# Performance work log

Measured on AMD Instinct MI355X. Metric: run time of the kernel, lower is better.

Reference implementation:

```python
import jax, jax.numpy as jnp
import numpy as np
import math

PERIODS = [4, 2, 1]          # period_num[-3:] sorted desc
SEQ, PRED, CH = 192, 96, 8
TOPM, DM = 20, 512
N_TRAIN, BSZ = 10000, 32


def decompose_mg(data):
    # data: [N, L, C] -> mg: [P, N, L, C], offset-removed (last step per period)
    N, L, C = data.shape
    mgs = []
    for g in PERIODS:
        cur = data.reshape(N, L // g, g, C).mean(axis=2)   # pooled
        cur = jnp.repeat(cur, g, axis=1)                   # repeat_interleave
        mgs.append(cur)
    mg = jnp.stack(mgs, axis=0)                            # [P, N, L, C]
    offset = mg[:, :, -1:, :]
    return mg - offset


def l2norm(x, eps=1e-12):
    n = jnp.sqrt(jnp.sum(x * x, axis=-1, keepdims=True))
    return x / jnp.maximum(n, eps)


def setup_inputs() -> dict:
    key = jax.random.key(0)
    ks = jax.random.split(key, 10)
    F = SEQ * CH
    return {
        "x": jax.random.normal(ks[0], (BSZ, SEQ, CH), dtype=jnp.float32),
        "index": jax.random.randint(ks[1], (BSZ,), 0, N_TRAIN),
        "train_data_all": jax.random.normal(ks[2], (N_TRAIN, SEQ, CH), dtype=jnp.float32),
        "y_data_all": jax.random.normal(ks[3], (N_TRAIN, PRED, CH), dtype=jnp.float32),
        "W_sim": jax.random.normal(ks[4], (F, F), dtype=jnp.float32) / math.sqrt(F),
        "b_sim": jax.random.normal(ks[5], (F,), dtype=jnp.float32) * 0.01,
        "Wq": jax.random.normal(ks[6], (CH, DM), dtype=jnp.float32) / math.sqrt(CH),
        "bq": jax.random.normal(ks[7], (DM,), dtype=jnp.float32) * 0.01,
        "Wk": jax.random.normal(ks[8], (CH, DM), dtype=jnp.float32) / math.sqrt(CH),
        "bk": jax.random.normal(ks[9], (DM,), dtype=jnp.float32) * 0.01,
    }


def reference(x, index, train_data_all, y_data_all, W_sim, b_sim, Wq, bq, Wk, bk):
    P = len(PERIODS)
    bsz = x.shape[0]
    n_train = train_data_all.shape[0]

    # multi-period decomposition (prepare_dataset + retrieve)
    train_mg = decompose_mg(train_data_all)   # [P, N, SEQ, CH]
    y_mg = decompose_mg(y_data_all)           # [P, N, PRED, CH]
    x_mg = decompose_mg(x)                    # [P, B, SEQ, CH]

    # periodic_batch_corr: shared linear then cosine similarity
    bx = x_mg.reshape(P, bsz, -1) @ W_sim + b_sim           # [P, B, F]
    ax = train_mg.reshape(P, n_train, -1) @ W_sim + b_sim   # [P, N, F]
    sim = jnp.einsum('pbf,pnf->pbn', l2norm(bx), l2norm(ax))

    # self-exclusion sliding mask (train=True)
    win = 2 * (SEQ + PRED) - 1
    slid = jnp.arange(win)[None, :] + (index - SEQ - PRED + 1)[:, None]
    slid = jnp.clip(slid, 0, n_train - 1)
    mask = jnp.zeros((bsz, n_train), dtype=bool).at[
        jnp.arange(bsz)[:, None], slid].set(True)
    sim = jnp.where(mask[None], -jnp.inf, sim)

    # top-m retrieval
    _, topm_idx = jax.lax.top_k(sim, TOPM)                  # [P, B, TOPM]

    # gather neighbors per period
    gather = jax.vmap(lambda src, i: src[i])                # over period axis
    k = gather(train_mg, topm_idx)                          # [P, B, M, SEQ, CH]
    v = gather(y_mg, topm_idx)                              # [P, B, M, PRED, CH]

    # cross attention (shared projections across periods)
    q_emb = x_mg @ Wq + bq                                  # [P, B, S, D]
    k_emb = k @ Wk + bk                                     # [P, B, M, T, D]
    scores = jnp.einsum('pbsd,pbmtd->pbsmt', q_emb, k_emb) / math.sqrt(DM)
    S = scores.shape[2]
    w = jax.nn.softmax(scores.reshape(P, bsz, S, TOPM * S), axis=-1)
    w = w.reshape(P, bsz, S, TOPM, S)
    nw = w.sum(axis=-1).sum(axis=2)                         # [P, B, M]
    nw = jax.nn.softmax(nw, axis=-1)
    out = jnp.einsum('pbm,pbmlc->pblc', nw, v)              # [P, B, PRED, CH]
    return out
```

## Files before the change

kernel.cpp:

```cpp
#include <hip/hip_runtime.h>
#include <hip/hip_bf16.h>
#include <math.h>

#define NPER 3
#define SEQL 192
#define PREDL 96
#define CH 8
#define FD 1536
#define NT 10000
#define BS 32
#define PB 96
#define TOPM 20
#define DM 512
#define HALFW 287
#define NROWS 30000
#define NRP2 10112
#define NRB2 79
#define NCB 12
#define PCOLS 24
#define NWG2 (NRB2*NCB)
#define NJ 3840
#define K0R 384
#define K1R 768
#define K2R 1536
#define KS 16
#define KSD 8
#define RSQRT_DM 0.04419417382415922f

typedef __attribute__((ext_vector_type(8))) short bf16x8;
typedef __attribute__((ext_vector_type(4))) float f32x4;
typedef __attribute__((address_space(3))) short lds_short_t;
typedef __attribute__((address_space(1))) const short glb_short_t;

__device__ inline float bflo(unsigned u){ return __uint_as_float(u << 16); }
__device__ inline float bfhi(unsigned u){ return __uint_as_float(u & 0xFFFF0000u); }
__device__ inline float bf2f(unsigned short u){ return __uint_as_float((unsigned)u << 16); }
__device__ inline unsigned short f2bf(float v){
  __hip_bfloat16 h = __float2bfloat16(v);
  return *reinterpret_cast<unsigned short*>(&h);
}

template<int L>
__global__ __launch_bounds__(256) void k_decompose(const float* __restrict__ data,
                                                   float* __restrict__ mg,
                                                   __hip_bfloat16* __restrict__ m0,
                                                   __hip_bfloat16* __restrict__ m1,
                                                   __hip_bfloat16* __restrict__ m2,
                                                   int N) {
  __shared__ float row[L*CH];
  __shared__ float m4[(L/4)*CH];
  __shared__ float m2s[(L/2)*CH];
  int n = blockIdx.x;
  const float* src = data + (size_t)n*L*CH;
  for (int e = threadIdx.x; e < L*CH/4; e += 256)
    *reinterpret_cast<float4*>(&row[e*4]) = *reinterpret_cast<const float4*>(&src[e*4]);
  __syncthreads();
  for (int i = threadIdx.x; i < (L/4)*CH; i += 256) {
    int j = i >> 3, c = i & 7;
    m4[i] = (row[(4*j)*CH+c] + row[(4*j+1)*CH+c] + row[(4*j+2)*CH+c] + row[(4*j+3)*CH+c]) * 0.25f;
  }
  for (int i = threadIdx.x; i < (L/2)*CH; i += 256) {
    int j = i >> 3, c = i & 7;
    m2s[i] = (row[(2*j)*CH+c] + row[(2*j+1)*CH+c]) * 0.5f;
  }
  __syncthreads();
  if (mg) {
    size_t plane = (size_t)N*L*CH;
    size_t base  = (size_t)n*L*CH;
    for (int e = threadIdx.x; e < L*CH/4; e += 256) {
      int i = e*4;
      int l = i >> 3, c0 = i & 7;
      float v0[4], v1[4], v2[4];
      #pragma unroll
      for (int j=0;j<4;j++) {
        int c = c0 + j;
        v0[j] = m4[(l>>2)*CH+c] - m4[(L/4-1)*CH+c];
        v1[j] = m2s[(l>>1)*CH+c] - m2s[(L/2-1)*CH+c];
        v2[j] = row[i+j] - row[(L-1)*CH+c];
      }
      *reinterpret_cast<float4*>(&mg[base+i])           = make_float4(v0[0],v0[1],v0[2],v0[3]);
      *reinterpret_cast<float4*>(&mg[plane+base+i])     = make_float4(v1[0],v1[1],v1[2],v1[3]);
      *reinterpret_cast<float4*>(&mg[2*plane+base+i])   = make_float4(v2[0],v2[1],v2[2],v2[3]);
    }
  }
  if (m0) {
    unsigned short* p0 = (unsigned short*)m0 + (size_t)n*K0R;
    unsigned short* p1 = (unsigned short*)m1 + (size_t)n*K1R;
    unsigned short* p2 = (unsigned short*)m2 + (size_t)n*K2R;
    for (int e = threadIdx.x; e < K0R/4; e += 256) {
      int i = e*4, c0 = i & 7;
      ushort4 u;
      u.x = f2bf(m4[i]   - m4[(L/4-1)*CH + c0]);
      u.y = f2bf(m4[i+1] - m4[(L/4-1)*CH + c0+1]);
      u.z = f2bf(m4[i+2] - m4[(L/4-1)*CH + c0+2]);
      u.w = f2bf(m4[i+3] - m4[(L/4-1)*CH + c0+3]);
      *reinterpret_cast<ushort4*>(&p0[i]) = u;
    }
    for (int e = threadIdx.x; e < K1R/4; e += 256) {
      int i = e*4, c0 = i & 7;
      ushort4 u;
      u.x = f2bf(m2s[i]   - m2s[(L/2-1)*CH + c0]);
      u.y = f2bf(m2s[i+1] - m2s[(L/2-1)*CH + c0+1]);
      u.z = f2bf(m2s[i+2] - m2s[(L/2-1)*CH + c0+2]);
      u.w = f2bf(m2s[i+3] - m2s[(L/2-1)*CH + c0+3]);
      *reinterpret_cast<ushort4*>(&p1[i]) = u;
    }
    for (int e = threadIdx.x; e < K2R/4; e += 256) {
      int i = e*4, c0 = i & 7;
      ushort4 u;
      u.x = f2bf(row[i]   - row[(L-1)*CH + c0]);
      u.y = f2bf(row[i+1] - row[(L-1)*CH + c0+1]);
      u.z = f2bf(row[i+2] - row[(L-1)*CH + c0+2]);
      u.w = f2bf(row[i+3] - row[(L-1)*CH + c0+3]);
      *reinterpret_cast<ushort4*>(&p2[i]) = u;
    }
  }
}

__global__ __launch_bounds__(256) void k_split(const float* __restrict__ src,
                                               __hip_bfloat16* __restrict__ H,
                                               __hip_bfloat16* __restrict__ L,
                                               int total4) {
  unsigned short* h = (unsigned short*)H;
  unsigned short* l = (unsigned short*)L;
  for (int e = blockIdx.x*256 + threadIdx.x; e < total4; e += gridDim.x*256) {
    float4 v = reinterpret_cast<const float4*>(src)[e];
    ushort4 uh, ul;
    uh.x = f2bf(v.x); ul.x = f2bf(v.x - bf2f(uh.x));
    uh.y = f2bf(v.y); ul.y = f2bf(v.y - bf2f(uh.y));
    uh.z = f2bf(v.z); ul.z = f2bf(v.z - bf2f(uh.z));
    uh.w = f2bf(v.w); ul.w = f2bf(v.w - bf2f(uh.w));
    *reinterpret_cast<ushort4*>(&h[e*4]) = uh;
    *reinterpret_cast<ushort4*>(&l[e*4]) = ul;
  }
}

__global__ __launch_bounds__(256) void k_wtg_all(const float* __restrict__ W,
                                                 __hip_bfloat16* __restrict__ wt0,
                                                 __hip_bfloat16* __restrict__ wt1,
                                                 __hip_bfloat16* __restrict__ wt2) {
  __shared__ float t[128][33];
  int bx = blockIdx.x;
  int G, kr0, Kred;
  __hip_bfloat16* Wt;
  if (bx < 12)      { G = 4; kr0 = bx*32;      Kred = K0R; Wt = wt0; }
  else if (bx < 36) { G = 2; kr0 = (bx-12)*32; Kred = K1R; Wt = wt1; }
  else              { G = 1; kr0 = (bx-36)*32; Kred = K2R; Wt = wt2; }
  int f0 = blockIdx.y*32;
  int k0 = kr0*G;
  int tid = threadIdx.x, tx = tid & 31, ty = tid >> 5;
  for (int i = ty; i < 32*G; i += 8)
    t[i][tx] = W[(size_t)(k0+i)*FD + f0 + tx];
  __syncthreads();
  for (int fl = ty; fl < 32; fl += 8) {
    float s = 0.f;
    for (int i=0;i<G;i++) s += t[((tx>>3)*G+i)*8 + (tx&7)][fl];
    Wt[(size_t)(f0+fl)*Kred + kr0 + tx] = __float2bfloat16(s);
  }
}

__global__ __launch_bounds__(256) void k_bx_part(const float* __restrict__ xmg,
                                                 const float* __restrict__ W,
                                                 float* __restrict__ bxp) {
  __shared__ float xs[PB][17];
  __shared__ float Ws[16][65];
  int f0 = blockIdx.x * 64;
  int ks = blockIdx.y;
  int kbase = ks * (FD/KS);
  int tid = threadIdx.x;
  int fl = tid & 63, gp = tid >> 6;
  float acc[24];
  #pragma unroll
  for (int j=0;j<24;j++) acc[j]=0.f;
  for (int k0 = kbase; k0 < kbase + FD/KS; k0 += 16) {
    for (int e = tid; e < PB*16; e += 256) {
      int r = e >> 4, k = e & 15;
      xs[r][k] = xmg[(size_t)r*FD + k0 + k];
    }
    for (int e = tid; e < 16*64; e += 256) {
      int k = e >> 6, f = e & 63;
      Ws[k][f] = W[(size_t)(k0+k)*FD + f0 + f];
    }
    __syncthreads();
    #pragma unroll
    for (int kk = 0; kk < 16; kk++) {
      float w = Ws[kk][fl];
      #pragma unroll
      for (int j=0;j<24;j++) acc[j] += w * xs[gp + 4*j][kk];
    }
    __syncthreads();
  }
  #pragma unroll
  for (int j=0;j<24;j++) {
    int pb = gp + 4*j;
    bxp[((size_t)ks*PB + pb)*FD + f0 + fl] = acc[j];
  }
}

__global__ __launch_bounds__(256) void k_bxnorm(const float* __restrict__ bxp,
                                                const float* __restrict__ bsim,
                                                float* __restrict__ u_out,
                                                float* __restrict__ cpb) {
  __shared__ float rowv[FD];
  __shared__ float r1[256], r2[256];
  __shared__ float invs;
  int pb = blockIdx.x, tid = threadIdx.x;
  float s2 = 0.f, sb = 0.f;
  for (int f = tid; f < FD; f += 256) {
    float s = 0.f;
    #pragma unroll
    for (int ks=0; ks<KS; ks++) s += bxp[((size_t)ks*PB + pb)*FD + f];
    s += bsim[f];
    rowv[f] = s;
    s2 += s*s; sb += s*bsim[f];
  }
  r1[tid]=s2; r2[tid]=sb; __syncthreads();
  for (int off=128; off>0; off>>=1) {
    if (tid<off) { r1[tid]+=r1[tid+off]; r2[tid]+=r2[tid+off]; }
    __syncthreads();
  }
  if (tid==0) {
    float iv = 1.f / fmaxf(sqrtf(r1[0]), 1e-12f);
    invs = iv;
    cpb[pb] = r2[0] * iv;
  }
  __syncthreads();
  float iv = invs;
  for (int f = tid; f < FD; f += 256) u_out[(size_t)pb*FD + f] = rowv[f]*iv;
}

__global__ __launch_bounds__(256) void k_t_part(const float* __restrict__ u,
                                                const float* __restrict__ W,
                                                float* __restrict__ tp) {
  __shared__ float us[PB][17];
  __shared__ float Wt[64][17];
  int k0 = blockIdx.x * 64;
  int ks = blockIdx.y;
  int fbase = ks * (FD/KS);
  int tid = threadIdx.x;
  int kl = tid & 63, gp = tid >> 6;
  float acc[24];
  #pragma unroll
  for (int j=0;j<24;j++) acc[j]=0.f;
  for (int fc = fbase; fc < fbase + FD/KS; fc += 16) {
    for (int e = tid; e < PB*16; e += 256) {
      int r = e >> 4, f = e & 15;
      us[r][f] = u[(size_t)r*FD + fc + f];
    }
    for (int e = tid; e < 64*16; e += 256) {
      int k = e >> 4, f = e & 15;
      Wt[k][f] = W[(size_t)(k0+k)*FD + fc + f];
    }
    __syncthreads();
    #pragma unroll
    for (int ff = 0; ff < 16; ff++) {
      float w = Wt[kl][ff];
      #pragma unroll
      for (int j=0;j<24;j++) acc[j] += w * us[gp + 4*j][ff];
    }
    __syncthreads();
  }
  #pragma unroll
  for (int j=0;j<24;j++) {
    int pb = gp + 4*j;
    tp[((size_t)ks*PB + pb)*FD + k0 + kl] = acc[j];
  }
}

__global__ __launch_bounds__(192) void k_tred_adj(const float* __restrict__ tp,
                                                  __hip_bfloat16* __restrict__ tadjH,
                                                  __hip_bfloat16* __restrict__ tadjL) {
  __shared__ float ts[SEQL*CH];
  __shared__ float Tc[CH];
  int pb = blockIdx.x;
  int p = pb / BS;
  int g = (p==0) ? 4 : (p==1) ? 2 : 1;
  int l = threadIdx.x;
  #pragma unroll
  for (int c=0;c<CH;c++) {
    float s = 0.f;
    #pragma unroll
    for (int ks=0; ks<KS; ks++) s += tp[((size_t)ks*PB + pb)*FD + l*CH + c];
    ts[l*CH+c] = s;
  }
  __syncthreads();
  if (l < CH) {
    float s=0.f;
    for (int j=0;j<SEQL;j++) s += ts[j*CH+l];
    Tc[l] = s;
  }
  __syncthreads();
  int j0 = (l/g)*g;
  bool last = (j0 == SEQL-g);
  float ig = 1.f/(float)g;
  unsigned short* th = (unsigned short*)tadjH;
  unsigned short* tl = (unsigned short*)tadjL;
  #pragma unroll
  for (int c=0;c<CH;c++) {
    float s = 0.f;
    for (int jj=0;jj<g;jj++) s += ts[(j0+jj)*CH+c];
    float v = s*ig - (last ? Tc[c]*ig : 0.f);
    unsigned short hv = f2bf(v);
    th[(size_t)pb*FD + l*CH+c] = hv;
    tl[(size_t)pb*FD + l*CH+c] = f2bf(v - bf2f(hv));
  }
}

__global__ __launch_bounds__(256) void k_norm_mfma(
    const __hip_bfloat16* __restrict__ A0b, const __hip_bfloat16* __restrict__ A1b,
    const __hip_bfloat16* __restrict__ A2b,
    const __hip_bfloat16* __restrict__ B0b, const __hip_bfloat16* __restrict__ B1b,
    const __hip_bfloat16* __restrict__ B2b,
    const float* __restrict__ bsim, float* __restrict__ part) {
  __shared__ __align__(16) short lA[128*32];
  __shared__ __align__(16) short lB[128*32];
  int bid = blockIdx.x;
  int p, seg;
  if (bid < NWG2)        { p = 2; seg = bid; }
  else if (bid < 2*NWG2) { p = 1; seg = bid - NWG2; }
  else                   { p = 0; seg = bid - 2*NWG2; }
  const short* A = (const short*)(p==0 ? A0b : (p==1 ? A1b : A2b));
  const short* B = (const short*)(p==0 ? B0b : (p==1 ? B1b : B2b));
  int K = (p==0) ? K0R : ((p==1) ? K1R : K2R);
  int q = NWG2 >> 3, r = NWG2 & 7;
  int xcd = seg & 7, pos = seg >> 3;
  int wgid = (xcd < r ? xcd*(q+1) : r*(q+1) + (xcd-r)*q) + pos;
  int rb = wgid / NCB, cb = wgid - rb*NCB;
  int row0 = rb*128, col0 = cb*128;
  int tid = threadIdx.x, lane = tid & 63, wid = tid >> 6;
  int wr = (wid>>1)*64, wc = (wid&1)*64;

  size_t aoff[2], boff[2];
  int ldsb[2];
  #pragma unroll
  for (int i=0;i<2;i++) {
    int lrow = (wid*2+i)*16 + (lane>>2);
    int sl = lane & 3;
    int ss = (sl - lrow - (lrow>>2)) & 3;
    aoff[i] = (size_t)(row0 + lrow)*K + 8*ss;
    boff[i] = (size_t)(col0 + lrow)*K + 8*ss;
    ldsb[i] = (wid*2+i)*16*32;
  }

  f32x4 acc[4][4];
  #pragma unroll
  for (int m=0;m<4;m++)
    #pragma unroll
    for (int n=0;n<4;n++) acc[m][n] = (f32x4){0.f,0.f,0.f,0.f};

  int kslot = lane >> 4;
  for (int k0 = 0; k0 < K; k0 += 32) {
    #pragma unroll
    for (int i=0;i<2;i++) {
      __builtin_amdgcn_global_load_lds((glb_short_t*)(A + aoff[i] + k0),
                                       (lds_short_t*)&lA[ldsb[i]], 16, 0, 0);
      __builtin_amdgcn_global_load_lds((glb_short_t*)(B + boff[i] + k0),
                                       (lds_short_t*)&lB[ldsb[i]], 16, 0, 0);
    }
    __syncthreads();
    bf16x8 af[4], bfr[4];
    #pragma unroll
    for (int m=0;m<4;m++) {
      int rr = wr + m*16 + (lane&15);
      int s = (kslot + rr + (rr>>2)) & 3;
      af[m] = *(const bf16x8*)&lA[rr*32 + s*8];
    }
    #pragma unroll
    for (int n=0;n<4;n++) {
      int rr = wc + n*16 + (lane&15);
      int s = (kslot + rr + (rr>>2)) & 3;
      bfr[n] = *(const bf16x8*)&lB[rr*32 + s*8];
    }
    #pragma unroll
    for (int m=0;m<4;m++)
      #pragma unroll
      for (int n=0;n<4;n++)
        acc[m][n] = __builtin_amdgcn_mfma_f32_16x16x32_bf16(af[m], bfr[n], acc[m][n], 0, 0, 0);
    __syncthreads();
  }

  float bv[4];
  #pragma unroll
  for (int n=0;n<4;n++) bv[n] = bsim[col0 + wc + n*16 + (lane&15)];
  int pslot = cb*2 + (wid&1);
  #pragma unroll
  for (int m=0;m<4;m++) {
    #pragma unroll
    for (int j=0;j<4;j++) {
      float s = 0.f;
      #pragma unroll
      for (int n=0;n<4;n++) { float v = acc[m][n][j] + bv[n]; s += v*v; }
      s += __shfl_xor(s, 1); s += __shfl_xor(s, 2);
      s += __shfl_xor(s, 4); s += __shfl_xor(s, 8);
      if ((lane & 15) == 0) {
        int rr = row0 + wr + m*16 + (lane>>4)*4 + j;
        part[((size_t)p*NRP2 + rr)*PCOLS + pslot] = s;
      }
    }
  }
}

__global__ __launch_bounds__(256) void k_norm_red(const float* __restrict__ part,
                                                  float* __restrict__ norm2) {
  int r = blockIdx.x*256 + threadIdx.x;
  if (r < NROWS) {
    int p = r / NT, rr = r - p*NT;
    float s=0.f;
    #pragma unroll
    for (int cb=0; cb<PCOLS; cb++) s += part[((size_t)p*NRP2 + rr)*PCOLS + cb];
    norm2[r] = s;
  }
}

__global__ __launch_bounds__(256) void k_dot_mfma(
    const __hip_bfloat16* __restrict__ tadjHb, const __hip_bfloat16* __restrict__ tadjLb,
    const __hip_bfloat16* __restrict__ trHb, const __hip_bfloat16* __restrict__ trLb,
    float* __restrict__ dotp) {
  __shared__ __align__(16) short lAH[128*32];
  __shared__ __align__(16) short lAL[128*32];
  __shared__ __align__(16) short lBH[128*32];
  __shared__ __align__(16) short lBL[128*32];
  int bid = blockIdx.x;
  int ks = bid & 7, cbn = bid >> 3;
  int col0 = cbn * 128;
  int kbase = ks * (FD/KSD);
  int tid = threadIdx.x, lane = tid & 63, wid = tid >> 6;
  int wr = (wid>>1)*64, wc = (wid&1)*64;
  const short* AH = (const short*)tadjHb;
  const short* AL = (const short*)tadjLb;
  const short* BH = (const short*)trHb;
  const short* BL = (const short*)trLb;

  size_t aoff[2], boff[2];
  int ldsb[2];
  #pragma unroll
  for (int i=0;i<2;i++) {
    int lrow = (wid*2+i)*16 + (lane>>2);
    int sl = lane & 3;
    int ss = (sl - lrow - (lrow>>2)) & 3;
    aoff[i] = (size_t)lrow*FD + 8*ss;
    boff[i] = (size_t)(col0 + lrow)*FD + 8*ss;
    ldsb[i] = (wid*2+i)*16*32;
  }

  f32x4 acc[4][4];
  #pragma unroll
  for (int m=0;m<4;m++)
    #pragma unroll
    for (int n=0;n<4;n++) acc[m][n] = (f32x4){0.f,0.f,0.f,0.f};

  int kslot = lane >> 4;
  for (int k0 = kbase; k0 < kbase + FD/KSD; k0 += 32) {
    #pragma unroll
    for (int i=0;i<2;i++) {
      __builtin_amdgcn_global_load_lds((glb_short_t*)(AH + aoff[i] + k0),
                                       (lds_short_t*)&lAH[ldsb[i]], 16, 0, 0);
      __builtin_amdgcn_global_load_lds((glb_short_t*)(AL + aoff[i] + k0),
                                       (lds_short_t*)&lAL[ldsb[i]], 16, 0, 0);
      __builtin_amdgcn_global_load_lds((glb_short_t*)(BH + boff[i] + k0),
                                       (lds_short_t*)&lBH[ldsb[i]], 16, 0, 0);
      __builtin_amdgcn_global_load_lds((glb_short_t*)(BL + boff[i] + k0),
                                       (lds_short_t*)&lBL[ldsb[i]], 16, 0, 0);
    }
    __syncthreads();
    bf16x8 ah[4], al[4], bh[4], bl[4];
    #pragma unroll
    for (int m=0;m<4;m++) {
      int rr = wr + m*16 + (lane&15);
      int s = (kslot + rr + (rr>>2)) & 3;
      ah[m] = *(const bf16x8*)&lAH[rr*32 + s*8];
      al[m] = *(const bf16x8*)&lAL[rr*32 + s*8];
    }
    #pragma unroll
    for (int n=0;n<4;n++) {
      int rr = wc + n*16 + (lane&15);
      int s = (kslot + rr + (rr>>2)) & 3;
      bh[n] = *(const bf16x8*)&lBH[rr*32 + s*8];
      bl[n] = *(const bf16x8*)&lBL[rr*32 + s*8];
    }
    #pragma unroll
    for (int m=0;m<4;m++)
      #pragma unroll
      for (int n=0;n<4;n++) {
        acc[m][n] = __builtin_amdgcn_mfma_f32_16x16x32_bf16(ah[m], bh[n], acc[m][n], 0, 0, 0);
        acc[m][n] = __builtin_amdgcn_mfma_f32_16x16x32_bf16(ah[m], bl[n], acc[m][n], 0, 0, 0);
        acc[m][n] = __builtin_amdgcn_mfma_f32_16x16x32_bf16(al[m], bh[n], acc[m][n], 0, 0, 0);
      }
    __syncthreads();
  }

  #pragma unroll
  for (int m=0;m<4;m++) {
    int prow = wr + m*16 + (lane>>4)*4;
    if (prow >= PB) continue;
    #pragma unroll
    for (int n=0;n<4;n++) {
      int ncol = col0 + wc + n*16 + (lane&15);
      if (ncol >= NT) continue;
      #pragma unroll
      for (int j=0;j<4;j++) {
        dotp[((size_t)ks*PB + prow + j)*NT + ncol] = acc[m][n][j];
      }
    }
  }
}

__global__ __launch_bounds__(256) void k_topk(const float* __restrict__ dotp,
                                              const float* __restrict__ cpb,
                                              const float* __restrict__ norm2,
                                              const int* __restrict__ index,
                                              int* __restrict__ topm) {
  __shared__ float vals[NT];
  __shared__ float rv[4];
  __shared__ int   ri[4];
  int pb = blockIdx.x;
  int p = pb / BS, b = pb % BS;
  int tid = threadIdx.x;
  int lane = tid & 63, wv = tid >> 6;
  int idx = index[b];
  int bl = idx - HALFW; if (bl < 0) bl = 0;
  int bh = idx + HALFW; if (bh > NT-1) bh = NT-1;
  const float* n2 = norm2 + (size_t)p*NT;
  float cp = cpb[pb];
  for (int i = tid; i < NT; i += 256) {
    float d = 0.f;
    #pragma unroll
    for (int ks=0; ks<KSD; ks++) d += dotp[((size_t)ks*PB + pb)*NT + i];
    d += cp;
    float v = d / fmaxf(sqrtf(n2[i]), 1e-12f);
    if (i >= bl && i <= bh) v = -INFINITY;
    vals[i] = v;
  }
  __syncthreads();
  for (int it = 0; it < TOPM; it++) {
    float bv = -INFINITY; int bi = NT;
    for (int i = tid; i < NT; i += 256) {
      float v = vals[i];
      if (v > bv) { bv = v; bi = i; }
    }
    #pragma unroll
    for (int off=32; off>0; off>>=1) {
      float ov = __shfl_xor(bv, off);
      int   oi = __shfl_xor(bi, off);
      if (ov > bv || (ov == bv && oi < bi)) { bv = ov; bi = oi; }
    }
    if (lane == 0) { rv[wv] = bv; ri[wv] = bi; }
    __syncthreads();
    if (tid == 0) {
      float fv = rv[0]; int fi = ri[0];
      #pragma unroll
      for (int w2=1; w2<4; w2++) {
        if (rv[w2] > fv || (rv[w2] == fv && ri[w2] < fi)) { fv = rv[w2]; fi = ri[w2]; }
      }
      topm[pb*TOPM + it] = fi;
      vals[fi] = -INFINITY;
    }
    __syncthreads();
  }
}

__global__ __launch_bounds__(128) void k_consts(const float* __restrict__ Wq,
                                                const float* __restrict__ bq,
                                                const float* __restrict__ Wk,
                                                const float* __restrict__ bk,
                                                float* __restrict__ cst) {
  int t = threadIdx.x;
  if (t < 64) {
    int c = t >> 3, e = t & 7;
    float s = 0.f;
    for (int d=0; d<DM; d++) s += Wq[c*DM+d] * Wk[e*DM+d];
    cst[t] = s;
  } else if (t < 72) {
    int c = t - 64; float s=0.f;
    for (int d=0;d<DM;d++) s += Wq[c*DM+d]*bk[d];
    cst[t] = s;
  } else if (t < 80) {
    int e = t - 72; float s=0.f;
    for (int d=0;d<DM;d++) s += Wk[e*DM+d]*bq[d];
    cst[t] = s;
  } else if (t == 80) {
    float s=0.f;
    for (int d=0;d<DM;d++) s += bq[d]*bk[d];
    cst[80] = s;
  }
}

__global__ __launch_bounds__(256) void k_v(const float* __restrict__ ydata,
                                           const int* __restrict__ topm,
                                           float* __restrict__ vbuf) {
  __shared__ float row[PREDL*CH];
  __shared__ float m4[(PREDL/4)*CH];
  __shared__ float m2[(PREDL/2)*CH];
  int bm = blockIdx.x;
  int pb = bm / TOPM;
  int p = pb / BS;
  int n = topm[bm];
  int tid = threadIdx.x;
  const float* src = ydata + (size_t)n*PREDL*CH;
  for (int i=tid; i<PREDL*CH; i+=256) row[i]=src[i];
  __syncthreads();
  for (int i=tid; i<(PREDL/4)*CH; i+=256) {
    int j=i>>3, c=i&7;
    m4[i] = (row[(4*j)*CH+c]+row[(4*j+1)*CH+c]+row[(4*j+2)*CH+c]+row[(4*j+3)*CH+c])*0.25f;
  }
  for (int i=tid; i<(PREDL/2)*CH; i+=256) {
    int j=i>>3, c=i&7;
    m2[i] = (row[(2*j)*CH+c]+row[(2*j+1)*CH+c])*0.5f;
  }
  __syncthreads();
  float* dst = vbuf + (size_t)bm*PREDL*CH;
  for (int i=tid; i<PREDL*CH; i+=256) {
    int l=i>>3, c=i&7;
    float v;
    if (p==0)      v = m4[(l>>2)*CH+c] - m4[(PREDL/4-1)*CH+c];
    else if (p==1) v = m2[(l>>1)*CH+c] - m2[(PREDL/2-1)*CH+c];
    else           v = row[i] - row[(PREDL-1)*CH+c];
    dst[i] = v;
  }
}

__global__ __launch_bounds__(256) void k_scores(const __hip_bfloat16* __restrict__ m0,
                                                const __hip_bfloat16* __restrict__ m1,
                                                const __hip_bfloat16* __restrict__ m2,
                                                const int* __restrict__ topm,
                                                const float* __restrict__ xmg,
                                                const float* __restrict__ cst,
                                                float* __restrict__ nws) {
  __shared__ float sc[NJ];
  __shared__ int tl[TOPM];
  __shared__ float wred[8];
  __shared__ float lcst[81];
  int pb = blockIdx.x, sg = blockIdx.y;
  int p = pb / BS;
  int tid = threadIdx.x;
  int lane = tid & 63, wv = tid >> 6;
  if (tid < TOPM) tl[tid] = topm[pb*TOPM + tid];
  if (tid >= 32 && tid < 32+81) lcst[tid-32] = cst[tid-32];
  __syncthreads();
  const short* plane = (const short*)(p==0 ? m0 : (p==1 ? m1 : m2));
  int Kp = (p==0) ? K0R : ((p==1) ? K1R : K2R);
  int sh = (p==0) ? 2 : ((p==1) ? 1 : 0);
  uint4 kreg[15];
  #pragma unroll
  for (int u=0; u<15; u++) {
    int j = tid + u*256;
    int m = j / SEQL, t2 = j - m*SEQL;
    kreg[u] = *reinterpret_cast<const uint4*>(plane + (size_t)tl[m]*Kp + ((t2>>sh)<<3));
  }
  for (int s8 = 0; s8 < 8; s8++) {
    int s = sg*8 + s8;
    int qr = pb*SEQL + s;
    float4 qa = *reinterpret_cast<const float4*>(&xmg[(size_t)qr*8]);
    float4 qc = *reinterpret_cast<const float4*>(&xmg[(size_t)qr*8+4]);
    float xq[8] = {qa.x,qa.y,qa.z,qa.w,qc.x,qc.y,qc.z,qc.w};
    float q[8];
    #pragma unroll
    for (int e=0;e<8;e++) {
      float ss = lcst[72+e];
      #pragma unroll
      for (int c=0;c<8;c++) ss += xq[c]*lcst[c*8+e];
      q[e] = ss;
    }
    float qb_s = lcst[80];
    #pragma unroll
    for (int c=0;c<8;c++) qb_s += xq[c]*lcst[64+c];
    float ms[15];
    float lmax = -INFINITY;
    #pragma unroll
    for (int u=0; u<15; u++) {
      uint4 w = kreg[u];
      float s0 = qb_s;
      s0 += q[0]*bflo(w.x) + q[1]*bfhi(w.x);
      s0 += q[2]*bflo(w.y) + q[3]*bfhi(w.y);
      s0 += q[4]*bflo(w.z) + q[5]*bfhi(w.z);
      s0 += q[6]*bflo(w.w) + q[7]*bfhi(w.w);
      s0 *= RSQRT_DM;
      ms[u] = s0;
      lmax = fmaxf(lmax, s0);
    }
    #pragma unroll
    for (int off=32; off>0; off>>=1) lmax = fmaxf(lmax, __shfl_xor(lmax, off));
    if (lane==0) wred[wv] = lmax;
    __syncthreads();
    float mx = fmaxf(fmaxf(wred[0],wred[1]),fmaxf(wred[2],wred[3]));
    float lsum = 0.f;
    #pragma unroll
    for (int u=0;u<15;u++) {
      int j = tid + u*256;
      float e = __expf(ms[u]-mx);
      sc[j] = e;
      lsum += e;
    }
    #pragma unroll
    for (int off=32; off>0; off>>=1) lsum += __shfl_xor(lsum, off);
    if (lane==0) wred[4+wv] = lsum;
    __syncthreads();
    float invZ = 1.f / (wred[4]+wred[5]+wred[6]+wred[7]);
    for (int m = wv; m < TOPM; m += 4) {
      float v = sc[m*SEQL + lane] + sc[m*SEQL + lane + 64] + sc[m*SEQL + lane + 128];
      #pragma unroll
      for (int off=32; off>0; off>>=1) v += __shfl_xor(v, off);
      if (lane==0) nws[((size_t)pb*SEQL + s)*TOPM + m] = v * invZ;
    }
    __syncthreads();
  }
}

__global__ __launch_bounds__(256) void k_out(const float* __restrict__ nws,
                                             const float* __restrict__ vbuf,
                                             float* __restrict__ out) {
  __shared__ float nwp[TOPM];
  __shared__ float nwf[TOPM];
  int pb = blockIdx.x;
  int tid = threadIdx.x;
  if (tid < TOPM) {
    float s=0.f;
    for (int ss=0; ss<SEQL; ss++) s += nws[((size_t)pb*SEQL+ss)*TOPM + tid];
    nwp[tid] = s;
  }
  __syncthreads();
  if (tid==0) {
    float mx=-INFINITY;
    for (int m=0;m<TOPM;m++) mx=fmaxf(mx,nwp[m]);
    float Z=0.f;
    for (int m=0;m<TOPM;m++){ float e=expf(nwp[m]-mx); nwf[m]=e; Z+=e; }
    float iz=1.f/Z;
    for (int m=0;m<TOPM;m++) nwf[m]*=iz;
  }
  __syncthreads();
  for (int i=tid; i<PREDL*CH; i+=256) {
    float o=0.f;
    #pragma unroll
    for (int m=0;m<TOPM;m++) o += nwf[m]*vbuf[((size_t)pb*TOPM+m)*PREDL*CH + i];
    out[(size_t)pb*PREDL*CH + i] = o;
  }
}

extern "C" void kernel_launch(void* const* d_in, const int* in_sizes, int n_in,
                              void* d_out, int out_size, void* d_ws, size_t ws_size,
                              hipStream_t stream) {
  const float* x     = (const float*)d_in[0];
  const int*   index = (const int*)  d_in[1];
  const float* train = (const float*)d_in[2];
  const float* ydata = (const float*)d_in[3];
  const float* Wsim  = (const float*)d_in[4];
  const float* bsim  = (const float*)d_in[5];
  const float* Wq    = (const float*)d_in[6];
  const float* bq    = (const float*)d_in[7];
  const float* Wk    = (const float*)d_in[8];
  const float* bk    = (const float*)d_in[9];
  float* out = (float*)d_out;

  float* ws = (float*)d_ws;
  size_t off = 0;
  auto alloc = [&](size_t n)->float* { float* pp = ws + off; off += (n + 63) & ~(size_t)63; return pp; };
  __hip_bfloat16* m0b = (__hip_bfloat16*)alloc((size_t)NRP2*K0R/2);
  __hip_bfloat16* m1b = (__hip_bfloat16*)alloc((size_t)NRP2*K1R/2);
  __hip_bfloat16* m2b = (__hip_bfloat16*)alloc((size_t)NRP2*K2R/2);
  __hip_bfloat16* wt0 = (__hip_bfloat16*)alloc((size_t)FD*K0R/2);
  __hip_bfloat16* wt1 = (__hip_bfloat16*)alloc((size_t)FD*K1R/2);
  __hip_bfloat16* wt2 = (__hip_bfloat16*)alloc((size_t)FD*K2R/2);
  __hip_bfloat16* trH = (__hip_bfloat16*)alloc((size_t)NRP2*FD/2);
  __hip_bfloat16* trL = (__hip_bfloat16*)alloc((size_t)NRP2*FD/2);
  __hip_bfloat16* tadjH = (__hip_bfloat16*)alloc((size_t)128*FD/2);
  __hip_bfloat16* tadjL = (__hip_bfloat16*)alloc((size_t)128*FD/2);
  float* x_mg     = alloc((size_t)NPER*BS*FD);
  float* bx       = alloc((size_t)PB*FD);
  float* cpb      = alloc(PB);
  float* gpart    = alloc((size_t)KS*PB*FD);
  float* part     = alloc((size_t)NPER*NRP2*PCOLS);
  float* norm2    = alloc(NROWS);
  float* dotp     = alloc((size_t)KSD*PB*NT);
  int*   topm     = (int*)alloc(PB*TOPM);
  float* cst      = alloc(128);
  float* vbuf     = alloc((size_t)PB*TOPM*PREDL*CH);
  float* nws      = alloc((size_t)PB*SEQL*TOPM);
  if (off * sizeof(float) > ws_size) return;

  hipMemsetAsync((char*)m0b + (size_t)NT*K0R*2, 0, (size_t)(NRP2-NT)*K0R*2, stream);
  hipMemsetAsync((char*)m1b + (size_t)NT*K1R*2, 0, (size_t)(NRP2-NT)*K1R*2, stream);
  hipMemsetAsync((char*)m2b + (size_t)NT*K2R*2, 0, (size_t)(NRP2-NT)*K2R*2, stream);
  hipMemsetAsync((char*)trH + (size_t)NT*FD*2, 0, (size_t)(NRP2-NT)*FD*2, stream);
  hipMemsetAsync((char*)trL + (size_t)NT*FD*2, 0, (size_t)(NRP2-NT)*FD*2, stream);
  hipMemsetAsync((char*)tadjH + (size_t)PB*FD*2, 0, (size_t)(128-PB)*FD*2, stream);
  hipMemsetAsync((char*)tadjL + (size_t)PB*FD*2, 0, (size_t)(128-PB)*FD*2, stream);

  k_decompose<SEQL><<<BS, 256, 0, stream>>>(x, x_mg, nullptr, nullptr, nullptr, BS);
  k_decompose<SEQL><<<NT, 256, 0, stream>>>(train, nullptr, m0b, m1b, m2b, NT);
  k_split<<<2048, 256, 0, stream>>>(train, trH, trL, NT*FD/4);
  k_wtg_all<<<dim3(84, 48), 256, 0, stream>>>(Wsim, wt0, wt1, wt2);
  k_bx_part<<<dim3(24, KS), 256, 0, stream>>>(x_mg, Wsim, gpart);
  k_bxnorm<<<PB, 256, 0, stream>>>(gpart, bsim, bx, cpb);
  k_t_part<<<dim3(24, KS), 256, 0, stream>>>(bx, Wsim, gpart);
  k_tred_adj<<<PB, 192, 0, stream>>>(gpart, tadjH, tadjL);
  k_norm_mfma<<<3*NWG2, 256, 0, stream>>>(m0b, m1b, m2b, wt0, wt1, wt2, bsim, part);
  k_norm_red<<<(NROWS+255)/256, 256, 0, stream>>>(part, norm2);
  k_dot_mfma<<<NRB2*KSD, 256, 0, stream>>>(tadjH, tadjL, trH, trL, dotp);
  k_topk<<<PB, 256, 0, stream>>>(dotp, cpb, norm2, index, topm);
  k_consts<<<1, 128, 0, stream>>>(Wq, bq, Wk, bk, cst);
  k_v<<<PB*TOPM, 256, 0, stream>>>(ydata, topm, vbuf);
  k_scores<<<dim3(PB, 24), 256, 0, stream>>>(m0b, m1b, m2b, topm, x_mg, cst, nws);
  k_out<<<PB, 256, 0, stream>>>(nws, vbuf, out);
}
```

Before: 470.1 us.

## Fuse split and consts kernels, chunk top-k, dedupe scores, drop memsets

Several independent changes at once. The bf16 hi/lo split of the training data now happens inside the decompose kernel, and the projection-constant computation rides as an extra block of the weight-transpose kernel, which saves launches and a second full read of the training data. Top-k selection is split into four chunks per query with a small merge kernel, so 4x more workgroups share the serial argmax loop. The scores kernel is templated per period so it only evaluates unique pooled positions; this is valid because repeated values scale the softmax numerator and denominator by the same factor. The padding memsets are removed, which relies on padded rows never reaching valid outputs.

After: 436.9 us. -7.1%, faster.

```diff
diff --git a/kernel.cpp b/kernel.cpp
--- a/kernel.cpp
+++ b/kernel.cpp
@@ -25,6 +25,8 @@
 #define K2R 1536
 #define KS 16
 #define KSD 8
+#define NCH 4
+#define CHSZ (NT/NCH)
 #define RSQRT_DM 0.04419417382415922f
 
 typedef __attribute__((ext_vector_type(8))) short bf16x8;
@@ -46,6 +48,8 @@
                                                    __hip_bfloat16* __restrict__ m0,
                                                    __hip_bfloat16* __restrict__ m1,
                                                    __hip_bfloat16* __restrict__ m2,
+                                                   __hip_bfloat16* __restrict__ trH,
+                                                   __hip_bfloat16* __restrict__ trL,
                                                    int N) {
   __shared__ float row[L*CH];
   __shared__ float m4[(L/4)*CH];
@@ -115,32 +119,56 @@
       *reinterpret_cast<ushort4*>(&p2[i]) = u;
     }
   }
-}
-
-__global__ __launch_bounds__(256) void k_split(const float* __restrict__ src,
-                                               __hip_bfloat16* __restrict__ H,
-                                               __hip_bfloat16* __restrict__ L,
-                                               int total4) {
-  unsigned short* h = (unsigned short*)H;
-  unsigned short* l = (unsigned short*)L;
-  for (int e = blockIdx.x*256 + threadIdx.x; e < total4; e += gridDim.x*256) {
-    float4 v = reinterpret_cast<const float4*>(src)[e];
-    ushort4 uh, ul;
-    uh.x = f2bf(v.x); ul.x = f2bf(v.x - bf2f(uh.x));
-    uh.y = f2bf(v.y); ul.y = f2bf(v.y - bf2f(uh.y));
-    uh.z = f2bf(v.z); ul.z = f2bf(v.z - bf2f(uh.z));
-    uh.w = f2bf(v.w); ul.w = f2bf(v.w - bf2f(uh.w));
-    *reinterpret_cast<ushort4*>(&h[e*4]) = uh;
-    *reinterpret_cast<ushort4*>(&l[e*4]) = ul;
+  if (trH) {
+    unsigned short* h = (unsigned short*)trH + (size_t)n*L*CH;
+    unsigned short* l = (unsigned short*)trL + (size_t)n*L*CH;
+    for (int e = threadIdx.x; e < L*CH/4; e += 256) {
+      int i = e*4;
+      ushort4 uh, ul;
+      uh.x = f2bf(row[i]);   ul.x = f2bf(row[i]   - bf2f(uh.x));
+      uh.y = f2bf(row[i+1]); ul.y = f2bf(row[i+1] - bf2f(uh.y));
+      uh.z = f2bf(row[i+2]); ul.z = f2bf(row[i+2] - bf2f(uh.z));
+      uh.w = f2bf(row[i+3]); ul.w = f2bf(row[i+3] - bf2f(uh.w));
+      *reinterpret_cast<ushort4*>(&h[i]) = uh;
+      *reinterpret_cast<ushort4*>(&l[i]) = ul;
+    }
   }
 }
 
 __global__ __launch_bounds__(256) void k_wtg_all(const float* __restrict__ W,
                                                  __hip_bfloat16* __restrict__ wt0,
                                                  __hip_bfloat16* __restrict__ wt1,
-                                                 __hip_bfloat16* __restrict__ wt2) {
+                                                 __hip_bfloat16* __restrict__ wt2,
+                                                 const float* __restrict__ Wq,
+                                                 const float* __restrict__ bq,
+                                                 const float* __restrict__ Wk,
+                                                 const float* __restrict__ bk,
+                                                 float* __restrict__ cst) {
   __shared__ float t[128][33];
   int bx = blockIdx.x;
+  if (bx == 84) {
+    if (blockIdx.y != 0) return;
+    int tt = threadIdx.x;
+    if (tt < 64) {
+      int c = tt >> 3, e = tt & 7;
+      float s = 0.f;
+      for (int d=0; d<DM; d++) s += Wq[c*DM+d] * Wk[e*DM+d];
+      cst[tt] = s;
+    } else if (tt < 72) {
+      int c = tt - 64; float s=0.f;
+      for (int d=0;d<DM;d++) s += Wq[c*DM+d]*bk[d];
+      cst[tt] = s;
+    } else if (tt < 80) {
+      int e = tt - 72; float s=0.f;
+      for (int d=0;d<DM;d++) s += Wk[e*DM+d]*bq[d];
+      cst[tt] = s;
+    } else if (tt == 80) {
+      float s=0.f;
+      for (int d=0;d<DM;d++) s += bq[d]*bk[d];
+      cst[80] = s;
+    }
+    return;
+  }
   int G, kr0, Kred;
   __hip_bfloat16* Wt;
   if (bx < 12)      { G = 4; kr0 = bx*32;      Kred = K0R; Wt = wt0; }
@@ -505,36 +533,38 @@
   }
 }
 
-__global__ __launch_bounds__(256) void k_topk(const float* __restrict__ dotp,
-                                              const float* __restrict__ cpb,
-                                              const float* __restrict__ norm2,
-                                              const int* __restrict__ index,
-                                              int* __restrict__ topm) {
-  __shared__ float vals[NT];
+__global__ __launch_bounds__(256) void k_topk_part(const float* __restrict__ dotp,
+                                                   const float* __restrict__ cpb,
+                                                   const float* __restrict__ norm2,
+                                                   const int* __restrict__ index,
+                                                   float* __restrict__ cv,
+                                                   int* __restrict__ ci) {
+  __shared__ float vals[CHSZ];
   __shared__ float rv[4];
   __shared__ int   ri[4];
-  int pb = blockIdx.x;
-  int p = pb / BS, b = pb % BS;
-  int tid = threadIdx.x;
-  int lane = tid & 63, wv = tid >> 6;
+  int pb = blockIdx.x, ch = blockIdx.y;
+  int p = pb / BS, b = pb - p*BS;
+  int n0 = ch*CHSZ;
+  int tid = threadIdx.x, lane = tid & 63, wv = tid >> 6;
   int idx = index[b];
   int bl = idx - HALFW; if (bl < 0) bl = 0;
   int bh = idx + HALFW; if (bh > NT-1) bh = NT-1;
   const float* n2 = norm2 + (size_t)p*NT;
   float cp = cpb[pb];
-  for (int i = tid; i < NT; i += 256) {
+  for (int i = tid; i < CHSZ; i += 256) {
+    int n = n0 + i;
     float d = 0.f;
     #pragma unroll
-    for (int ks=0; ks<KSD; ks++) d += dotp[((size_t)ks*PB + pb)*NT + i];
+    for (int ks=0; ks<KSD; ks++) d += dotp[((size_t)ks*PB + pb)*NT + n];
     d += cp;
-    float v = d / fmaxf(sqrtf(n2[i]), 1e-12f);
-    if (i >= bl && i <= bh) v = -INFINITY;
+    float v = d / fmaxf(sqrtf(n2[n]), 1e-12f);
+    if (n >= bl && n <= bh) v = -INFINITY;
     vals[i] = v;
   }
   __syncthreads();
   for (int it = 0; it < TOPM; it++) {
-    float bv = -INFINITY; int bi = NT;
-    for (int i = tid; i < NT; i += 256) {
+    float bv = -INFINITY; int bi = CHSZ;
+    for (int i = tid; i < CHSZ; i += 256) {
       float v = vals[i];
       if (v > bv) { bv = v; bi = i; }
     }
@@ -549,39 +579,45 @@
     if (tid == 0) {
       float fv = rv[0]; int fi = ri[0];
       #pragma unroll
-      for (int w2=1; w2<4; w2++) {
+      for (int w2=1; w2<4; w2++)
         if (rv[w2] > fv || (rv[w2] == fv && ri[w2] < fi)) { fv = rv[w2]; fi = ri[w2]; }
-      }
-      topm[pb*TOPM + it] = fi;
+      cv[(pb*NCH + ch)*TOPM + it] = fv;
+      ci[(pb*NCH + ch)*TOPM + it] = n0 + fi;
       vals[fi] = -INFINITY;
     }
     __syncthreads();
   }
 }
 
-__global__ __launch_bounds__(128) void k_consts(const float* __restrict__ Wq,
-                                                const float* __restrict__ bq,
-                                                const float* __restrict__ Wk,
-                                                const float* __restrict__ bk,
-                                                float* __restrict__ cst) {
-  int t = threadIdx.x;
-  if (t < 64) {
-    int c = t >> 3, e = t & 7;
-    float s = 0.f;
-    for (int d=0; d<DM; d++) s += Wq[c*DM+d] * Wk[e*DM+d];
-    cst[t] = s;
-  } else if (t < 72) {
-    int c = t - 64; float s=0.f;
-    for (int d=0;d<DM;d++) s += Wq[c*DM+d]*bk[d];
-    cst[t] = s;
-  } else if (t < 80) {
-    int e = t - 72; float s=0.f;
-    for (int d=0;d<DM;d++) s += Wk[e*DM+d]*bq[d];
-    cst[t] = s;
-  } else if (t == 80) {
-    float s=0.f;
-    for (int d=0;d<DM;d++) s += bq[d]*bk[d];
-    cst[80] = s;
+__global__ __launch_bounds__(64) void k_topk_merge(const float* __restrict__ cv,
+                                                   const int* __restrict__ ci,
+                                                   int* __restrict__ topm) {
+  __shared__ float v[NCH*TOPM];
+  __shared__ int   id[NCH*TOPM];
+  int pb = blockIdx.x;
+  int lane = threadIdx.x;
+  for (int i = lane; i < NCH*TOPM; i += 64) {
+    v[i]  = cv[pb*NCH*TOPM + i];
+    id[i] = ci[pb*NCH*TOPM + i];
+  }
+  __syncthreads();
+  for (int it = 0; it < TOPM; it++) {
+    float bv = -INFINITY; int bi = 0x7fffffff;
+    for (int i = lane; i < NCH*TOPM; i += 64) {
+      float vv = v[i];
+      int ii = id[i];
+      if (vv > bv || (vv == bv && ii < bi)) { bv = vv; bi = ii; }
+    }
+    #pragma unroll
+    for (int off=32; off>0; off>>=1) {
+      float ov = __shfl_xor(bv, off);
+      int   oi = __shfl_xor(bi, off);
+      if (ov > bv || (ov == bv && oi < bi)) { bv = ov; bi = oi; }
+    }
+    if (lane == 0) topm[pb*TOPM + it] = bi;
+    for (int i = lane; i < NCH*TOPM; i += 64)
+      if (id[i] == bi) v[i] = -INFINITY;
+    __syncthreads();
   }
 }
 
@@ -619,6 +655,102 @@
   }
 }
 
+template<int SH>
+__device__ __forceinline__ void scores_body(
+    const short* __restrict__ plane, int Kp,
+    int pb, int sg,
+    const int* __restrict__ topm,
+    const float* __restrict__ xmg,
+    const float* __restrict__ cst,
+    float* __restrict__ nws,
+    float* sc, int* tl, float* wred, float* lcst) {
+  constexpr int UNQ = SEQL >> SH;
+  constexpr int J   = TOPM * UNQ;
+  constexpr int NU  = (J + 255) >> 8;
+  constexpr bool FULL = (J % 256 == 0);
+  int tid = threadIdx.x;
+  int lane = tid & 63, wv = tid >> 6;
+  if (tid < TOPM) tl[tid] = topm[pb*TOPM + tid];
+  if (tid >= 32 && tid < 32+81) lcst[tid-32] = cst[tid-32];
+  __syncthreads();
+  uint4 kreg[NU];
+  #pragma unroll
+  for (int u=0; u<NU; u++) {
+    int j = tid + u*256;
+    if (FULL || j < J) {
+      int m = j / UNQ, jj = j - m*UNQ;
+      kreg[u] = *reinterpret_cast<const uint4*>(plane + (size_t)tl[m]*Kp + jj*8);
+    }
+  }
+  for (int s8 = 0; s8 < 8; s8++) {
+    int s = sg*8 + s8;
+    int qr = pb*SEQL + s;
+    float4 qa = *reinterpret_cast<const float4*>(&xmg[(size_t)qr*8]);
+    float4 qc = *reinterpret_cast<const float4*>(&xmg[(size_t)qr*8+4]);
+    float xq[8] = {qa.x,qa.y,qa.z,qa.w,qc.x,qc.y,qc.z,qc.w};
+    float q[8];
+    #pragma unroll
+    for (int e=0;e<8;e++) {
+      float ss = lcst[72+e];
+      #pragma unroll
+      for (int c=0;c<8;c++) ss += xq[c]*lcst[c*8+e];
+      q[e] = ss;
+    }
+    float qb_s = lcst[80];
+    #pragma unroll
+    for (int c=0;c<8;c++) qb_s += xq[c]*lcst[64+c];
+    float ms[NU];
+    float lmax = -INFINITY;
+    #pragma unroll
+    for (int u=0; u<NU; u++) {
+      int j = tid + u*256;
+      if (FULL || j < J) {
+        uint4 w = kreg[u];
+        float s0 = qb_s;
+        s0 += q[0]*bflo(w.x) + q[1]*bfhi(w.x);
+        s0 += q[2]*bflo(w.y) + q[3]*bfhi(w.y);
+        s0 += q[4]*bflo(w.z) + q[5]*bfhi(w.z);
+        s0 += q[6]*bflo(w.w) + q[7]*bfhi(w.w);
+        s0 *= RSQRT_DM;
+        ms[u] = s0;
+        lmax = fmaxf(lmax, s0);
+      } else ms[u] = -INFINITY;
+    }
+    #pragma unroll
+    for (int off=32; off>0; off>>=1) lmax = fmaxf(lmax, __shfl_xor(lmax, off));
+    if (lane==0) wred[wv] = lmax;
+    __syncthreads();
+    float mx = fmaxf(fmaxf(wred[0],wred[1]),fmaxf(wred[2],wred[3]));
+    float lsum = 0.f;
+    #pragma unroll
+    for (int u=0; u<NU; u++) {
+      int j = tid + u*256;
+      if (FULL || j < J) {
+        float e = __expf(ms[u]-mx);
+        sc[j] = e;
+        lsum += e;
+      }
+    }
+    #pragma unroll
+    for (int off=32; off>0; off>>=1) lsum += __shfl_xor(lsum, off);
+    if (lane==0) wred[4+wv] = lsum;
+    __syncthreads();
+    float invZ = 1.f / (wred[4]+wred[5]+wred[6]+wred[7]);
+    for (int m = wv; m < TOPM; m += 4) {
+      float v = 0.f;
+      #pragma unroll
+      for (int jj = 0; jj < UNQ; jj += 64) {
+        int j2 = jj + lane;
+        if (UNQ % 64 == 0 || j2 < UNQ) v += sc[m*UNQ + j2];
+      }
+      #pragma unroll
+      for (int off=32; off>0; off>>=1) v += __shfl_xor(v, off);
+      if (lane==0) nws[((size_t)pb*SEQL + s)*TOPM + m] = v * invZ;
+    }
+    __syncthreads();
+  }
+}
+
 __global__ __launch_bounds__(256) void k_scores(const __hip_bfloat16* __restrict__ m0,
                                                 const __hip_bfloat16* __restrict__ m1,
                                                 const __hip_bfloat16* __restrict__ m2,
@@ -632,78 +764,12 @@
   __shared__ float lcst[81];
   int pb = blockIdx.x, sg = blockIdx.y;
   int p = pb / BS;
-  int tid = threadIdx.x;
-  int lane = tid & 63, wv = tid >> 6;
-  if (tid < TOPM) tl[tid] = topm[pb*TOPM + tid];
-  if (tid >= 32 && tid < 32+81) lcst[tid-32] = cst[tid-32];
-  __syncthreads();
-  const short* plane = (const short*)(p==0 ? m0 : (p==1 ? m1 : m2));
-  int Kp = (p==0) ? K0R : ((p==1) ? K1R : K2R);
-  int sh = (p==0) ? 2 : ((p==1) ? 1 : 0);
-  uint4 kreg[15];
-  #pragma unroll
-  for (int u=0; u<15; u++) {
-    int j = tid + u*256;
-    int m = j / SEQL, t2 = j - m*SEQL;
-    kreg[u] = *reinterpret_cast<const uint4*>(plane + (size_t)tl[m]*Kp + ((t2>>sh)<<3));
-  }
-  for (int s8 = 0; s8 < 8; s8++) {
-    int s = sg*8 + s8;
-    int qr = pb*SEQL + s;
-    float4 qa = *reinterpret_cast<const float4*>(&xmg[(size_t)qr*8]);
-    float4 qc = *reinterpret_cast<const float4*>(&xmg[(size_t)qr*8+4]);
-    float xq[8] = {qa.x,qa.y,qa.z,qa.w,qc.x,qc.y,qc.z,qc.w};
-    float q[8];
-    #pragma unroll
-    for (int e=0;e<8;e++) {
-      float ss = lcst[72+e];
-      #pragma unroll
-      for (int c=0;c<8;c++) ss += xq[c]*lcst[c*8+e];
-      q[e] = ss;
-    }
-    float qb_s = lcst[80];
-    #pragma unroll
-    for (int c=0;c<8;c++) qb_s += xq[c]*lcst[64+c];
-    float ms[15];
-    float lmax = -INFINITY;
-    #pragma unroll
-    for (int u=0; u<15; u++) {
-      uint4 w = kreg[u];
-      float s0 = qb_s;
-      s0 += q[0]*bflo(w.x) + q[1]*bfhi(w.x);
-      s0 += q[2]*bflo(w.y) + q[3]*bfhi(w.y);
-      s0 += q[4]*bflo(w.z) + q[5]*bfhi(w.z);
-      s0 += q[6]*bflo(w.w) + q[7]*bfhi(w.w);
-      s0 *= RSQRT_DM;
-      ms[u] = s0;
-      lmax = fmaxf(lmax, s0);
-    }
-    #pragma unroll
-    for (int off=32; off>0; off>>=1) lmax = fmaxf(lmax, __shfl_xor(lmax, off));
-    if (lane==0) wred[wv] = lmax;
-    __syncthreads();
-    float mx = fmaxf(fmaxf(wred[0],wred[1]),fmaxf(wred[2],wred[3]));
-    float lsum = 0.f;
-    #pragma unroll
-    for (int u=0;u<15;u++) {
-      int j = tid + u*256;
-      float e = __expf(ms[u]-mx);
-      sc[j] = e;
-      lsum += e;
-    }
-    #pragma unroll
-    for (int off=32; off>0; off>>=1) lsum += __shfl_xor(lsum, off);
-    if (lane==0) wred[4+wv] = lsum;
-    __syncthreads();
-    float invZ = 1.f / (wred[4]+wred[5]+wred[6]+wred[7]);
-    for (int m = wv; m < TOPM; m += 4) {
-      float v = sc[m*SEQL + lane] + sc[m*SEQL + lane + 64] + sc[m*SEQL + lane + 128];
-      #pragma unroll
-      for (int off=32; off>0; off>>=1) v += __shfl_xor(v, off);
-      if (lane==0) nws[((size_t)pb*SEQL + s)*TOPM + m] = v * invZ;
-    }
-    __syncthreads();
-  }
+  if (p == 0)
+    scores_body<2>((const short*)m0, K0R, pb, sg, topm, xmg, cst, nws, sc, tl, wred, lcst);
+  else if (p == 1)
+    scores_body<1>((const short*)m1, K1R, pb, sg, topm, xmg, cst, nws, sc, tl, wred, lcst);
+  else
+    scores_body<0>((const short*)m2, K2R, pb, sg, topm, xmg, cst, nws, sc, tl, wred, lcst);
 }
 
 __global__ __launch_bounds__(256) void k_out(const float* __restrict__ nws,
@@ -771,24 +837,19 @@
   float* part     = alloc((size_t)NPER*NRP2*PCOLS);
   float* norm2    = alloc(NROWS);
   float* dotp     = alloc((size_t)KSD*PB*NT);
+  float* cv       = alloc((size_t)PB*NCH*TOPM);
+  int*   ci       = (int*)alloc(PB*NCH*TOPM);
   int*   topm     = (int*)alloc(PB*TOPM);
   float* cst      = alloc(128);
   float* vbuf     = alloc((size_t)PB*TOPM*PREDL*CH);
   float* nws      = alloc((size_t)PB*SEQL*TOPM);
   if (off * sizeof(float) > ws_size) return;
 
-  hipMemsetAsync((char*)m0b + (size_t)NT*K0R*2, 0, (size_t)(NRP2-NT)*K0R*2, stream);
-  hipMemsetAsync((char*)m1b + (size_t)NT*K1R*2, 0, (size_t)(NRP2-NT)*K1R*2, stream);
-  hipMemsetAsync((char*)m2b + (size_t)NT*K2R*2, 0, (size_t)(NRP2-NT)*K2R*2, stream);
-  hipMemsetAsync((char*)trH + (size_t)NT*FD*2, 0, (size_t)(NRP2-NT)*FD*2, stream);
-  hipMemsetAsync((char*)trL + (size_t)NT*FD*2, 0, (size_t)(NRP2-NT)*FD*2, stream);
-  hipMemsetAsync((char*)tadjH + (size_t)PB*FD*2, 0, (size_t)(128-PB)*FD*2, stream);
-  hipMemsetAsync((char*)tadjL + (size_t)PB*FD*2, 0, (size_t)(128-PB)*FD*2, stream);
-
-  k_decompose<SEQL><<<BS, 256, 0, stream>>>(x, x_mg, nullptr, nullptr, nullptr, BS);
-  k_decompose<SEQL><<<NT, 256, 0, stream>>>(train, nullptr, m0b, m1b, m2b, NT);
-  k_split<<<2048, 256, 0, stream>>>(train, trH, trL, NT*FD/4);
-  k_wtg_all<<<dim3(84, 48), 256, 0, stream>>>(Wsim, wt0, wt1, wt2);
+  k_decompose<SEQL><<<BS, 256, 0, stream>>>(x, x_mg, nullptr, nullptr, nullptr,
+                                            nullptr, nullptr, BS);
+  k_decompose<SEQL><<<NT, 256, 0, stream>>>(train, nullptr, m0b, m1b, m2b,
+                                            trH, trL, NT);
+  k_wtg_all<<<dim3(85, 48), 256, 0, stream>>>(Wsim, wt0, wt1, wt2, Wq, bq, Wk, bk, cst);
   k_bx_part<<<dim3(24, KS), 256, 0, stream>>>(x_mg, Wsim, gpart);
   k_bxnorm<<<PB, 256, 0, stream>>>(gpart, bsim, bx, cpb);
   k_t_part<<<dim3(24, KS), 256, 0, stream>>>(bx, Wsim, gpart);
@@ -796,8 +857,8 @@
   k_norm_mfma<<<3*NWG2, 256, 0, stream>>>(m0b, m1b, m2b, wt0, wt1, wt2, bsim, part);
   k_norm_red<<<(NROWS+255)/256, 256, 0, stream>>>(part, norm2);
   k_dot_mfma<<<NRB2*KSD, 256, 0, stream>>>(tadjH, tadjL, trH, trL, dotp);
-  k_topk<<<PB, 256, 0, stream>>>(dotp, cpb, norm2, index, topm);
-  k_consts<<<1, 128, 0, stream>>>(Wq, bq, Wk, bk, cst);
+  k_topk_part<<<dim3(PB, NCH), 256, 0, stream>>>(dotp, cpb, norm2, index, cv, ci);
+  k_topk_merge<<<PB, 64, 0, stream>>>(cv, ci, topm);
   k_v<<<PB*TOPM, 256, 0, stream>>>(ydata, topm, vbuf);
   k_scores<<<dim3(PB, 24), 256, 0, stream>>>(m0b, m1b, m2b, topm, x_mg, cst, nws);
   k_out<<<PB, 256, 0, stream>>>(nws, vbuf, out);
```
